# Kernel tuning notes

Hardware: AMD Instinct MI355X
Metric: run time of the kernel (lower is better)

Reference implementation:

```python
import jax, jax.numpy as jnp
import numpy as np

B, K, D = 128, 64, 1536        # batch, image regions, CNN feature dim
EM, H, A = 512, 1024, 1024     # embedding, hidden, attention dims
VOCAB, MAX_LEN = 10000, 30


def setup_inputs() -> dict:
    key = jax.random.key(0)
    ks = jax.random.split(key, 20)
    def p(i, shape):
        return jax.random.normal(ks[i], shape, dtype=jnp.float32) * 0.02
    z = lambda *s: jnp.zeros(s, jnp.float32)
    return {
        "im_input": jax.random.normal(ks[0], (B, K, D), dtype=jnp.float32),
        "w_input": jax.random.randint(ks[1], (B, MAX_LEN + 1), 0, VOCAB),
        "caption_lengths": jax.random.randint(ks[2], (B,), 2, MAX_LEN + 2),
        "emb": p(3, (VOCAB, EM)),
        "W_enc": p(4, (D, H)), "b_enc": z(H),
        "W_glob": p(5, (D, EM)), "b_glob": z(EM),
        "W_ih": p(6, (2 * EM, 4 * H)), "b_ih": z(4 * H),
        "W_hh": p(7, (H, 4 * H)), "b_hh": z(4 * H),
        "W_xg": p(8, (2 * EM, H)), "b_xg": z(H),
        "W_hg": p(9, (H, H)), "b_hg": z(H),
        "Wv": p(10, (H, A)), "bv": z(A),
        "Ws": p(11, (H, A)), "bs": z(A),
        "Wh": p(12, (H, A)), "bh": z(A),
        "wa": p(13, (A, 1)), "ba": z(1),
        "W_out": p(14, (H, VOCAB)), "b_out": z(VOCAB),
    }


def _forward(im_input, emb, W_enc, b_enc, W_glob, b_glob, W_ih, b_ih, W_hh, b_hh,
             W_xg, b_xg, W_hg, b_hg, Wv, bv, Ws, bs, Wh, bh, wa, ba, W_out, b_out,
             w_input, caption_lengths):
    # ImageEncoder: per-region features (B,K,H) and global feature (B,EM)
    V = jax.nn.relu(jnp.einsum('bkd,dh->bkh', im_input, W_enc) + b_enc)
    g = jax.nn.relu(jnp.mean(im_input, axis=1) @ W_glob + b_glob)
    # sort batch by caption length, descending (as in the torch forward)
    order = jnp.argsort(-caption_lengths)
    w = w_input[order]
    g = g[order]
    V = V[order]
    lens = caption_lengths[order] - 1  # has_end_seq_token=True
    target = w[:, 1:]
    h0 = jnp.zeros((B, H), jnp.float32)
    c0 = jnp.zeros((B, H), jnp.float32)

    # Full-batch scan is math-equivalent to the dynamic batch_size_t slicing:
    # lengths are sorted descending, so rows that go inactive never become
    # active again; their masked predictions stay zero, matching the original.
    def step(carry, t):
        h, c = carry
        x = jnp.concatenate([emb[w[:, t]], g], axis=1)  # (B, 2*EM)
        # SentinelLSTM: standard LSTM cell + visual sentinel gate
        gates = x @ W_ih + b_ih + h @ W_hh + b_hh
        i_g, f_g, g_g, o_g = jnp.split(gates, 4, axis=1)
        c_new = jax.nn.sigmoid(f_g) * c + jax.nn.sigmoid(i_g) * jnp.tanh(g_g)
        h_new = jax.nn.sigmoid(o_g) * jnp.tanh(c_new)
        s = jax.nn.sigmoid(x @ W_xg + b_xg + h @ W_hg + b_hg) * jnp.tanh(c_new)
        # Adaptive attention over K regions + sentinel
        hp = h_new @ Wh + bh                                      # (B,A)
        zv = (jnp.tanh(V @ Wv + bv + hp[:, None, :]) @ wa)[..., 0] + ba  # (B,K)
        zs = jnp.tanh(s @ Ws + bs + hp) @ wa + ba                  # (B,1)
        alpha = jax.nn.softmax(jnp.concatenate([zv, zs], axis=1), axis=1)  # (B,K+1)
        ctx = jnp.einsum('bk,bkh->bh', alpha[:, :-1], V)
        beta = alpha[:, -1:]
        z_t = beta * s + (1.0 - beta) * ctx + h_new
        # MultimodalDecoder (decoding_stack_size=1 -> single projection)
        probs = jax.nn.softmax(z_t @ W_out + b_out, axis=1)        # (B,VOCAB)
        probs = jnp.where((t < lens)[:, None], probs, 0.0)
        return (h_new, c_new), probs

    _, P = jax.lax.scan(step, (h0, c0), jnp.arange(MAX_LEN))
    predictions = jnp.transpose(P, (1, 0, 2))  # (B, MAX_LEN, VOCAB)
    return predictions, target, lens


def reference(im_input, w_input, caption_lengths, emb, W_enc, b_enc, W_glob, b_glob,
              W_ih, b_ih, W_hh, b_hh, W_xg, b_xg, W_hg, b_hg, Wv, bv, Ws, bs,
              Wh, bh, wa, ba, W_out, b_out):
    return _forward(im_input, emb, W_enc, b_enc, W_glob, b_glob, W_ih, b_ih,
                    W_hh, b_hh, W_xg, b_xg, W_hg, b_hg, Wv, bv, Ws, bs, Wh, bh,
                    wa, ba, W_out, b_out, w_input, caption_lengths)
```

## Files before the change

kernel.cpp:

```cpp
#include <hip/hip_runtime.h>
#include <math.h>

#define NB 128
#define NKK 64
#define ND 1536
#define NEM 512
#define NH 1024
#define NVOC 10000
#define NT 30
#define CHT 6

#define BM 128
#define BN 64
#define BK 64

typedef __bf16 bf16x8 __attribute__((ext_vector_type(8)));
typedef __bf16 bf16x4 __attribute__((ext_vector_type(4)));
typedef float f32x4 __attribute__((ext_vector_type(4)));

__device__ __forceinline__ float ftanh(float x) {
    float e = __expf(2.f * x);
    return 1.f - 2.f * __builtin_amdgcn_rcpf(e + 1.f);
}
__device__ __forceinline__ float fsig(float x) {
    return __builtin_amdgcn_rcpf(1.f + __expf(-x));
}

__global__ void sort_kernel(const int* __restrict__ cap, const int* __restrict__ w,
                            float* __restrict__ out_target, float* __restrict__ out_lens,
                            int* __restrict__ order, int* __restrict__ lens_s,
                            int* __restrict__ widx) {
    __shared__ int lcap[NB];
    __shared__ int sord[NB];
    int b = threadIdx.x;
    lcap[b] = cap[b];
    __syncthreads();
    int lb = lcap[b];
    int pos = 0;
    for (int j = 0; j < NB; j++) {
        int lj = lcap[j];
        if (lj > lb || (lj == lb && j < b)) pos++;
    }
    sord[pos] = b;
    __syncthreads();
    int src = sord[b];
    order[b] = src;
    int ln = lcap[src] - 1;
    lens_s[b] = ln;
    out_lens[b] = (float)ln;
    for (int j = 0; j < NT; j++)
        out_target[b * NT + j] = (float)w[src * (NT + 1) + j + 1];
    for (int t = 0; t < NT; t++)
        widx[t * NB + b] = w[src * (NT + 1) + t];
}

__global__ void init_kernel(float* __restrict__ c, float* __restrict__ ghh0,
                            float* __restrict__ ghh1) {
    int tid = blockIdx.x * 256 + threadIdx.x;
    if (tid < NB * NH) c[tid] = 0.f;
    if (tid < NB * 5120) { ghh0[tid] = 0.f; ghh1[tid] = 0.f; }
}

__global__ void meanim_kernel(const float* __restrict__ im, const int* __restrict__ order,
                              __bf16* __restrict__ meanb) {
    int b = blockIdx.x;
    int src = order[b];
    const float* base = im + (size_t)src * NKK * ND;
    for (int d = threadIdx.x; d < ND; d += 256) {
        float acc = 0.f;
        for (int k = 0; k < NKK; k++) acc += base[(size_t)k * ND + d];
        meanb[b * ND + d] = (__bf16)(acc * (1.0f / NKK));
    }
}

__global__ void conv_perm_kernel(const float* __restrict__ im, const int* __restrict__ order,
                                 __bf16* __restrict__ imb) {
    int e8 = blockIdx.x * 256 + threadIdx.x;
    size_t elem = (size_t)e8 * 8;
    int bp = (int)(elem / (NKK * ND));
    size_t rem = elem % (NKK * ND);
    const float* src = im + (size_t)order[bp] * NKK * ND + rem;
    float4 f0 = *(const float4*)(src);
    float4 f1 = *(const float4*)(src + 4);
    bf16x8 v = {(__bf16)f0.x, (__bf16)f0.y, (__bf16)f0.z, (__bf16)f0.w,
                (__bf16)f1.x, (__bf16)f1.y, (__bf16)f1.z, (__bf16)f1.w};
    *(bf16x8*)(imb + elem) = v;
}

__global__ __launch_bounds__(256) void transpose_pack(
    const float* __restrict__ src, int ldn, int K, int N,
    __bf16* __restrict__ dst, int ldk) {
    __shared__ float tile[64][65];
    int k0 = blockIdx.y * 64, n0 = blockIdx.x * 64;
    int t = threadIdx.x;
    int kr = t >> 2, nc0 = (t & 3) * 16;
    int kk = k0 + kr;
#pragma unroll
    for (int j = 0; j < 16; j += 4) {
        int nn = n0 + nc0 + j;
        float4 v = make_float4(0.f, 0.f, 0.f, 0.f);
        if (kk < K && nn + 3 < N) v = *(const float4*)(src + (size_t)kk * ldn + nn);
        else if (kk < K) {
            float tmp[4] = {0.f, 0.f, 0.f, 0.f};
            for (int q = 0; q < 4; q++) if (nn + q < N) tmp[q] = src[(size_t)kk * ldn + nn + q];
            v = make_float4(tmp[0], tmp[1], tmp[2], tmp[3]);
        }
        tile[kr][nc0 + j + 0] = v.x; tile[kr][nc0 + j + 1] = v.y;
        tile[kr][nc0 + j + 2] = v.z; tile[kr][nc0 + j + 3] = v.w;
    }
    __syncthreads();
    int nr = t >> 2, kc0 = (t & 3) * 16;
    if (n0 + nr < N) {
        __bf16* drow = dst + (size_t)(n0 + nr) * ldk + k0 + kc0;
#pragma unroll
        for (int j = 0; j < 16; j++)
            if (k0 + kc0 + j < K) drow[j] = (__bf16)tile[kc0 + j][nr];
    }
}

__global__ void conv_bf16_vec(const float* __restrict__ src, __bf16* __restrict__ dst, int n4) {
    int id = blockIdx.x * 256 + threadIdx.x;
    if (id < n4) {
        float4 v = *(const float4*)(src + (size_t)id * 4);
        __bf16* d = dst + (size_t)id * 4;
        d[0] = (__bf16)v.x; d[1] = (__bf16)v.y; d[2] = (__bf16)v.z; d[3] = (__bf16)v.w;
    }
}

__global__ void pack_biases(const float* __restrict__ b_ih, const float* __restrict__ b_hh,
                            const float* __restrict__ b_xg, const float* __restrict__ b_hg,
                            const float* __restrict__ bh, const float* __restrict__ bs,
                            float* __restrict__ bstep, float* __restrict__ b2) {
    int i = blockIdx.x * 256 + threadIdx.x;
    if (i < 4096) bstep[i] = b_ih[i] + b_hh[i];
    else bstep[i] = b_xg[i - 4096] + b_hg[i - 4096];
    if (i < 1024) b2[i] = bh[i];
    else if (i < 2048) b2[i] = bs[i - 1024];
}

template <int AMODE, bool RELU, bool OUTBF>
__global__ __launch_bounds__(256) void gemm_k(
    const void* __restrict__ Aptr, int lda,
    const __bf16* __restrict__ Bt, int ldb,
    const float* __restrict__ bias,
    void* __restrict__ Cptr, int ldc,
    int N, int K,
    const int* __restrict__ widx,
    const __bf16* __restrict__ embb, const __bf16* __restrict__ gbf,
    int swz, size_t sA, size_t sB, size_t sBias, size_t sC) {
    const int t = threadIdx.x;
    const int lane = t & 63;
    const int wid = t >> 6;
    const int wr = wid >> 1, wc = wid & 1;
    int bx = blockIdx.x, by = blockIdx.y;
    if (swz == 1) {
        int L = by * gridDim.x + bx;
        int xcd = L & 7, q = L >> 3;
        by = xcd * (gridDim.y >> 3) + q / gridDim.x;
        bx = q % gridDim.x;
    } else if (swz == 3) {
        int total = gridDim.x * gridDim.y;
        int L = by * gridDim.x + bx;
        int xcd = L & 7, idx = L >> 3;
        int newL = xcd * (total >> 3) + idx;
        by = newL / gridDim.x;
        bx = newL % gridDim.x;
    }
    const int z = blockIdx.z;
    const int m0 = by * BM;
    const int n0 = bx * BN;
    const int lr = lane & 15, lg = lane >> 4, lr8 = lr & 7;

    __shared__ __bf16 As[BM * BK];
    __shared__ __bf16 Bs[BN * BK];

    f32x4 acc[4][2];
#pragma unroll
    for (int i = 0; i < 4; i++)
#pragma unroll
        for (int j = 0; j < 2; j++) acc[i][j] = (f32x4){0.f, 0.f, 0.f, 0.f};

    const int s_row = t >> 1;
    const int s_g0 = (t & 1) * 4;
    const int s_col = t >> 2;
    const int s_bg0 = (t & 3) * 2;
    const int r8 = s_row & 7, c8 = s_col & 7;
    const int aw0 = (s_row << 6) + (((s_g0 + 0) ^ r8) << 3);
    const int aw1 = (s_row << 6) + (((s_g0 + 1) ^ r8) << 3);
    const int aw2 = (s_row << 6) + (((s_g0 + 2) ^ r8) << 3);
    const int aw3 = (s_row << 6) + (((s_g0 + 3) ^ r8) << 3);
    const int bw0 = (s_col << 6) + (((s_bg0 + 0) ^ c8) << 3);
    const int bw1 = (s_col << 6) + (((s_bg0 + 1) ^ c8) << 3);
    const int rA0 = (wr * 64 + 0 * 16 + lr) << 6;
    const int rA1 = (wr * 64 + 1 * 16 + lr) << 6;
    const int rA2 = (wr * 64 + 2 * 16 + lr) << 6;
    const int rA3 = (wr * 64 + 3 * 16 + lr) << 6;
    const int cB0 = (wc * 32 + 0 * 16 + lr) << 6;
    const int cB1 = (wc * 32 + 1 * 16 + lr) << 6;

    const __bf16* a_srcb = nullptr;
    const __bf16* e_base = nullptr;
    const __bf16* g_base = nullptr;
    if (AMODE == 1) {
        int r = m0 + s_row;
        e_base = embb + (size_t)widx[r] * NEM + s_g0 * 8;
        g_base = gbf + (size_t)(r & 127) * NEM + s_g0 * 8 - NEM;
    } else {
        a_srcb = (const __bf16*)Aptr + z * sA + (size_t)(m0 + s_row) * lda + s_g0 * 8;
    }
    const __bf16* b_src = Bt + z * sB + (size_t)(n0 + s_col) * ldb + s_bg0 * 8;
    const bool b_ok = (n0 + s_col) < N;

    auto loadA = [&](int k0, bf16x8& a0, bf16x8& a1, bf16x8& a2, bf16x8& a3) {
        if (AMODE == 1) {
            int kk = k0 + s_g0 * 8;
            const bf16x8* p = (const bf16x8*)((kk < NEM ? e_base : g_base) + k0);
            a0 = p[0]; a1 = p[1]; a2 = p[2]; a3 = p[3];
        } else {
            const bf16x8* p = (const bf16x8*)(a_srcb + k0);
            a0 = p[0]; a1 = p[1]; a2 = p[2]; a3 = p[3];
        }
    };
    auto loadB = [&](int k0, bf16x8& b0, bf16x8& b1) {
        if (b_ok) {
            const bf16x8* p = (const bf16x8*)(b_src + k0);
            b0 = p[0]; b1 = p[1];
        } else {
            bf16x8 zv = {};
            b0 = zv; b1 = zv;
        }
    };
    auto writeS = [&](bf16x8 a0, bf16x8 a1, bf16x8 a2, bf16x8 a3, bf16x8 b0, bf16x8 b1) {
        *(bf16x8*)&As[aw0] = a0; *(bf16x8*)&As[aw1] = a1;
        *(bf16x8*)&As[aw2] = a2; *(bf16x8*)&As[aw3] = a3;
        *(bf16x8*)&Bs[bw0] = b0; *(bf16x8*)&Bs[bw1] = b1;
    };
    auto compute = [&]() {
#pragma unroll
        for (int ks = 0; ks < 2; ks++) {
            const int gsw = ((ks * 4 + lg) ^ lr8) << 3;
            bf16x8 af0 = *(const bf16x8*)&As[rA0 + gsw];
            bf16x8 af1 = *(const bf16x8*)&As[rA1 + gsw];
            bf16x8 af2 = *(const bf16x8*)&As[rA2 + gsw];
            bf16x8 af3 = *(const bf16x8*)&As[rA3 + gsw];
            bf16x8 bv0 = *(const bf16x8*)&Bs[cB0 + gsw];
            bf16x8 bv1 = *(const bf16x8*)&Bs[cB1 + gsw];
            acc[0][0] = __builtin_amdgcn_mfma_f32_16x16x32_bf16(af0, bv0, acc[0][0], 0, 0, 0);
            acc[0][1] = __builtin_amdgcn_mfma_f32_16x16x32_bf16(af0, bv1, acc[0][1], 0, 0, 0);
            acc[1][0] = __builtin_amdgcn_mfma_f32_16x16x32_bf16(af1, bv0, acc[1][0], 0, 0, 0);
            acc[1][1] = __builtin_amdgcn_mfma_f32_16x16x32_bf16(af1, bv1, acc[1][1], 0, 0, 0);
            acc[2][0] = __builtin_amdgcn_mfma_f32_16x16x32_bf16(af2, bv0, acc[2][0], 0, 0, 0);
            acc[2][1] = __builtin_amdgcn_mfma_f32_16x16x32_bf16(af2, bv1, acc[2][1], 0, 0, 0);
            acc[3][0] = __builtin_amdgcn_mfma_f32_16x16x32_bf16(af3, bv0, acc[3][0], 0, 0, 0);
            acc[3][1] = __builtin_amdgcn_mfma_f32_16x16x32_bf16(af3, bv1, acc[3][1], 0, 0, 0);
        }
    };

    bf16x8 a0, a1, a2, a3, b0, b1;
    bf16x8 c0, c1, c2, c3, d0, d1;
    loadA(0, a0, a1, a2, a3);
    loadB(0, b0, b1);
    for (int k0 = 0; k0 < K; k0 += 2 * BK) {
        writeS(a0, a1, a2, a3, b0, b1);
        __syncthreads();
        loadA(k0 + BK, c0, c1, c2, c3);
        loadB(k0 + BK, d0, d1);
        compute();
        __syncthreads();
        writeS(c0, c1, c2, c3, d0, d1);
        __syncthreads();
        if (k0 + 2 * BK < K) {
            loadA(k0 + 2 * BK, a0, a1, a2, a3);
            loadB(k0 + 2 * BK, b0, b1);
        }
        compute();
        __syncthreads();
    }

    const float* bias_z = bias + z * sBias;
    float* Cf = (float*)Cptr + z * sC;
    __bf16* Cb = (__bf16*)Cptr + z * sC;
#pragma unroll
    for (int mi = 0; mi < 4; mi++) {
#pragma unroll
        for (int ni = 0; ni < 2; ni++) {
            int col = n0 + wc * 32 + ni * 16 + lr;
            if (col < N) {
                float bb = bias_z[col];
#pragma unroll
                for (int rr = 0; rr < 4; rr++) {
                    int row = m0 + wr * 64 + mi * 16 + lg * 4 + rr;
                    float v = acc[mi][ni][rr] + bb;
                    if (RELU) v = fmaxf(v, 0.f);
                    if (OUTBF) Cb[(size_t)row * ldc + col] = (__bf16)v;
                    else Cf[(size_t)row * ldc + col] = v;
                }
            }
        }
    }
}

__device__ __forceinline__ void step_gemm(
    __bf16* As, __bf16* Bs,
    const __bf16* __restrict__ Ab, int lda,
    const __bf16* __restrict__ Bt, int ldb,
    const float* __restrict__ bias,
    float* __restrict__ C, int ldc, int N, int n0, int K) {
    const int t = threadIdx.x;
    const int lane = t & 63;
    const int wid = t >> 6;
    const int wr = wid >> 1, wc = wid & 1;
    const int lr = lane & 15, lg = lane >> 4, lr8 = lr & 7;

    f32x4 acc[4][2];
#pragma unroll
    for (int i = 0; i < 4; i++)
#pragma unroll
        for (int j = 0; j < 2; j++) acc[i][j] = (f32x4){0.f, 0.f, 0.f, 0.f};

    const int s_row = t >> 1;
    const int s_g0 = (t & 1) * 4;
    const int s_col = t >> 2;
    const int s_bg0 = (t & 3) * 2;
    const int r8 = s_row & 7, c8 = s_col & 7;
    const int aw0 = (s_row << 6) + (((s_g0 + 0) ^ r8) << 3);
    const int aw1 = (s_row << 6) + (((s_g0 + 1) ^ r8) << 3);
    const int aw2 = (s_row << 6) + (((s_g0 + 2) ^ r8) << 3);
    const int aw3 = (s_row << 6) + (((s_g0 + 3) ^ r8) << 3);
    const int bw0 = (s_col << 6) + (((s_bg0 + 0) ^ c8) << 3);
    const int bw1 = (s_col << 6) + (((s_bg0 + 1) ^ c8) << 3);
    const int rA0 = (wr * 64 + 0 * 16 + lr) << 6;
    const int rA1 = (wr * 64 + 1 * 16 + lr) << 6;
    const int rA2 = (wr * 64 + 2 * 16 + lr) << 6;
    const int rA3 = (wr * 64 + 3 * 16 + lr) << 6;
    const int cB0 = (wc * 32 + 0 * 16 + lr) << 6;
    const int cB1 = (wc * 32 + 1 * 16 + lr) << 6;

    const __bf16* a_src = Ab + (size_t)s_row * lda + s_g0 * 8;
    const __bf16* b_src = Bt + (size_t)(n0 + s_col) * ldb + s_bg0 * 8;
    const bool b_ok = (n0 + s_col) < N;

    auto loadA = [&](int k0, bf16x8& a0, bf16x8& a1, bf16x8& a2, bf16x8& a3) {
        const bf16x8* p = (const bf16x8*)(a_src + k0);
        a0 = p[0]; a1 = p[1]; a2 = p[2]; a3 = p[3];
    };
    auto loadB = [&](int k0, bf16x8& b0, bf16x8& b1) {
        if (b_ok) {
            const bf16x8* p = (const bf16x8*)(b_src + k0);
            b0 = p[0]; b1 = p[1];
        } else {
            bf16x8 zv = {};
            b0 = zv; b1 = zv;
        }
    };
    auto writeS = [&](bf16x8 a0, bf16x8 a1, bf16x8 a2, bf16x8 a3, bf16x8 b0, bf16x8 b1) {
        *(bf16x8*)&As[aw0] = a0; *(bf16x8*)&As[aw1] = a1;
        *(bf16x8*)&As[aw2] = a2; *(bf16x8*)&As[aw3] = a3;
        *(bf16x8*)&Bs[bw0] = b0; *(bf16x8*)&Bs[bw1] = b1;
    };
    auto compute = [&]() {
#pragma unroll
        for (int ks = 0; ks < 2; ks++) {
            const int gsw = ((ks * 4 + lg) ^ lr8) << 3;
            bf16x8 af0 = *(const bf16x8*)&As[rA0 + gsw];
            bf16x8 af1 = *(const bf16x8*)&As[rA1 + gsw];
            bf16x8 af2 = *(const bf16x8*)&As[rA2 + gsw];
            bf16x8 af3 = *(const bf16x8*)&As[rA3 + gsw];
            bf16x8 bv0 = *(const bf16x8*)&Bs[cB0 + gsw];
            bf16x8 bv1 = *(const bf16x8*)&Bs[cB1 + gsw];
            acc[0][0] = __builtin_amdgcn_mfma_f32_16x16x32_bf16(af0, bv0, acc[0][0], 0, 0, 0);
            acc[0][1] = __builtin_amdgcn_mfma_f32_16x16x32_bf16(af0, bv1, acc[0][1], 0, 0, 0);
            acc[1][0] = __builtin_amdgcn_mfma_f32_16x16x32_bf16(af1, bv0, acc[1][0], 0, 0, 0);
            acc[1][1] = __builtin_amdgcn_mfma_f32_16x16x32_bf16(af1, bv1, acc[1][1], 0, 0, 0);
            acc[2][0] = __builtin_amdgcn_mfma_f32_16x16x32_bf16(af2, bv0, acc[2][0], 0, 0, 0);
            acc[2][1] = __builtin_amdgcn_mfma_f32_16x16x32_bf16(af2, bv1, acc[2][1], 0, 0, 0);
            acc[3][0] = __builtin_amdgcn_mfma_f32_16x16x32_bf16(af3, bv0, acc[3][0], 0, 0, 0);
            acc[3][1] = __builtin_amdgcn_mfma_f32_16x16x32_bf16(af3, bv1, acc[3][1], 0, 0, 0);
        }
    };

    bf16x8 a0, a1, a2, a3, b0, b1;
    bf16x8 c0, c1, c2, c3, d0, d1;
    loadA(0, a0, a1, a2, a3);
    loadB(0, b0, b1);
    for (int k0 = 0; k0 < K; k0 += 2 * BK) {
        writeS(a0, a1, a2, a3, b0, b1);
        __syncthreads();
        loadA(k0 + BK, c0, c1, c2, c3);
        loadB(k0 + BK, d0, d1);
        compute();
        __syncthreads();
        writeS(c0, c1, c2, c3, d0, d1);
        __syncthreads();
        if (k0 + 2 * BK < K) {
            loadA(k0 + 2 * BK, a0, a1, a2, a3);
            loadB(k0 + 2 * BK, b0, b1);
        }
        compute();
        __syncthreads();
    }

#pragma unroll
    for (int mi = 0; mi < 4; mi++) {
#pragma unroll
        for (int ni = 0; ni < 2; ni++) {
            int col = n0 + wc * 32 + ni * 16 + lr;
            if (col < N) {
                float bb = bias ? bias[col] : 0.f;
#pragma unroll
                for (int rr = 0; rr < 4; rr++) {
                    int row = wr * 64 + mi * 16 + lg * 4 + rr;
                    C[(size_t)row * ldc + col] = acc[mi][ni][rr] + bb;
                }
            }
        }
    }
}

__global__ __launch_bounds__(256) void lstm_kernel(
    const __bf16* __restrict__ Xpre, const float* __restrict__ g0,
    const float* __restrict__ g1, float* __restrict__ c,
    __bf16* __restrict__ H_all, __bf16* __restrict__ S_all, int t) {
    int i4 = (blockIdx.x * 256 + threadIdx.x) * 4;
    int b = i4 >> 10, j = i4 & 1023;
    const __bf16* xp = Xpre + ((size_t)t * NB + b) * 5120 + j;
    const float* p0 = g0 + (size_t)b * 5120 + j;
    const float* p1 = g1 + (size_t)b * 5120 + j;
    bf16x4 xi = *(const bf16x4*)(xp);
    bf16x4 xf = *(const bf16x4*)(xp + 1024);
    bf16x4 xg = *(const bf16x4*)(xp + 2048);
    bf16x4 xo = *(const bf16x4*)(xp + 3072);
    bf16x4 xs = *(const bf16x4*)(xp + 4096);
    float4 gi0 = *(const float4*)(p0), gi1 = *(const float4*)(p1);
    float4 gf0 = *(const float4*)(p0 + 1024), gf1 = *(const float4*)(p1 + 1024);
    float4 gg0 = *(const float4*)(p0 + 2048), gg1 = *(const float4*)(p1 + 2048);
    float4 go0 = *(const float4*)(p0 + 3072), go1 = *(const float4*)(p1 + 3072);
    float4 gs0 = *(const float4*)(p0 + 4096), gs1 = *(const float4*)(p1 + 4096);
    float4 cv = *(const float4*)(c + i4);
    float ia[4] = {gi0.x + gi1.x, gi0.y + gi1.y, gi0.z + gi1.z, gi0.w + gi1.w};
    float fa[4] = {gf0.x + gf1.x, gf0.y + gf1.y, gf0.z + gf1.z, gf0.w + gf1.w};
    float ga[4] = {gg0.x + gg1.x, gg0.y + gg1.y, gg0.z + gg1.z, gg0.w + gg1.w};
    float oa[4] = {go0.x + go1.x, go0.y + go1.y, go0.z + go1.z, go0.w + go1.w};
    float sa[4] = {gs0.x + gs1.x, gs0.y + gs1.y, gs0.z + gs1.z, gs0.w + gs1.w};
    float cvp[4] = {cv.x, cv.y, cv.z, cv.w};
    float cn4[4];
    bf16x4 hv, sv;
#pragma unroll
    for (int e = 0; e < 4; e++) {
        float ig = fsig((float)xi[e] + ia[e]);
        float fg = fsig((float)xf[e] + fa[e]);
        float gv = ftanh((float)xg[e] + ga[e]);
        float og = fsig((float)xo[e] + oa[e]);
        float sg = fsig((float)xs[e] + sa[e]);
        float cn = fg * cvp[e] + ig * gv;
        float tc = ftanh(cn);
        cn4[e] = cn;
        hv[e] = (__bf16)(og * tc);
        sv[e] = (__bf16)(sg * tc);
    }
    *(float4*)(c + i4) = make_float4(cn4[0], cn4[1], cn4[2], cn4[3]);
    *(bf16x4*)(H_all + (size_t)t * NB * NH + i4) = hv;
    *(bf16x4*)(S_all + (size_t)t * NB * NH + i4) = sv;
}

__global__ __launch_bounds__(256) void gatesHH_kernel(
    const __bf16* __restrict__ H_t, const __bf16* __restrict__ Whh,
    float* __restrict__ g0, float* __restrict__ g1) {
    __shared__ __bf16 As[BM * BK];
    __shared__ __bf16 Bs[BN * BK];
    int kc = blockIdx.x & 1, n = blockIdx.x >> 1;
    step_gemm(As, Bs, H_t + kc * 512, NH, Whh + kc * 512, 2048, nullptr,
              kc == 0 ? g0 : g1, 5120, 5120, n * 64, 512);
}

__global__ __launch_bounds__(256) void attn_all_kernel(
    const __bf16* __restrict__ VA, const __bf16* __restrict__ V,
    const __bf16* __restrict__ HPa, const __bf16* __restrict__ SWSa,
    const float* __restrict__ wa, const __bf16* __restrict__ H_all,
    const __bf16* __restrict__ S_all, __bf16* __restrict__ Z_all) {
    __shared__ float zscore[NKK + 1];
    __shared__ float alpha_s[NKK + 1];
    int tb = blockIdx.x;
    int b = tb & 127;
    int wave = threadIdx.x >> 6, lane = threadIdx.x & 63;

    float hp_reg[16], wa_reg[16];
    {
        const bf16x8* hr = (const bf16x8*)(HPa + (size_t)tb * NH + lane * 16);
        bf16x8 h0 = hr[0], h1 = hr[1];
        const float* wb = wa + lane * 16;
#pragma unroll
        for (int q = 0; q < 4; q++) {
            float4 wv = *(const float4*)(wb + q * 4);
            wa_reg[q * 4 + 0] = wv.x; wa_reg[q * 4 + 1] = wv.y;
            wa_reg[q * 4 + 2] = wv.z; wa_reg[q * 4 + 3] = wv.w;
        }
#pragma unroll
        for (int j = 0; j < 8; j++) { hp_reg[j] = (float)h0[j]; hp_reg[8 + j] = (float)h1[j]; }
    }
    for (int k = wave; k <= NKK; k += 4) {
        float p = 0.f;
        if (k < NKK) {
            const bf16x8* row = (const bf16x8*)(VA + ((size_t)(b * NKK + k)) * NH + lane * 16);
            bf16x8 v0 = row[0], v1 = row[1];
#pragma unroll
            for (int j = 0; j < 8; j++) {
                p += ftanh((float)v0[j] + hp_reg[j]) * wa_reg[j];
                p += ftanh((float)v1[j] + hp_reg[8 + j]) * wa_reg[8 + j];
            }
        } else {
            const bf16x8* sr = (const bf16x8*)(SWSa + (size_t)tb * NH + lane * 16);
            bf16x8 s0 = sr[0], s1 = sr[1];
#pragma unroll
            for (int j = 0; j < 8; j++) {
                p += ftanh((float)s0[j] + hp_reg[j]) * wa_reg[j];
                p += ftanh((float)s1[j] + hp_reg[8 + j]) * wa_reg[8 + j];
            }
        }
        for (int off = 32; off; off >>= 1) p += __shfl_down(p, off);
        if (lane == 0) zscore[k] = p;
    }
    __syncthreads();
    if (threadIdx.x == 0) {
        float mx = zscore[0];
        for (int i = 1; i <= NKK; i++) mx = fmaxf(mx, zscore[i]);
        float ssum = 0.f;
        for (int i = 0; i <= NKK; i++) { float e = __expf(zscore[i] - mx); alpha_s[i] = e; ssum += e; }
        float inv = __builtin_amdgcn_rcpf(ssum);
        for (int i = 0; i <= NKK; i++) alpha_s[i] *= inv;
    }
    __syncthreads();
    float beta = alpha_s[NKK];
    {
        int jj0 = threadIdx.x * 4;
        const __bf16* vp = V + ((size_t)b * NKK) * NH + jj0;
        float c0 = 0.f, c1 = 0.f, c2 = 0.f, c3 = 0.f;
#pragma unroll 8
        for (int k = 0; k < NKK; k++) {
            bf16x4 vv = *(const bf16x4*)(vp + (size_t)k * NH);
            float a = alpha_s[k];
            c0 += a * (float)vv[0]; c1 += a * (float)vv[1];
            c2 += a * (float)vv[2]; c3 += a * (float)vv[3];
        }
        bf16x4 s4 = *(const bf16x4*)(S_all + (size_t)tb * NH + jj0);
        bf16x4 h4 = *(const bf16x4*)(H_all + (size_t)tb * NH + jj0);
        float ob = 1.f - beta;
        bf16x4 zv;
        zv[0] = (__bf16)(beta * (float)s4[0] + ob * c0 + (float)h4[0]);
        zv[1] = (__bf16)(beta * (float)s4[1] + ob * c1 + (float)h4[1]);
        zv[2] = (__bf16)(beta * (float)s4[2] + ob * c2 + (float)h4[2]);
        zv[3] = (__bf16)(beta * (float)s4[3] + ob * c3 + (float)h4[3]);
        *(bf16x4*)(Z_all + (size_t)tb * NH + jj0) = zv;
    }
}

__global__ __launch_bounds__(256) void softmax_chunk_kernel(
    const float* __restrict__ logitsC, const int* __restrict__ lens,
    float* __restrict__ pred, int t0) {
    __shared__ float se[NVOC];
    __shared__ float sred[4], sred2[4];
    int r = blockIdx.x;
    int tt = r >> 7, b = r & 127;
    int t = t0 + tt;
    float* out = pred + (size_t)b * NT * NVOC + (size_t)t * NVOC;
    if (t >= lens[b]) {
        for (int v = threadIdx.x; v < NVOC; v += 256) out[v] = 0.f;
        return;
    }
    const float* lg = logitsC + (size_t)r * NVOC;
    float mx = -1e30f;
    for (int v = threadIdx.x; v < NVOC; v += 256) {
        float x = lg[v];
        se[v] = x;
        mx = fmaxf(mx, x);
    }
    for (int off = 32; off; off >>= 1) mx = fmaxf(mx, __shfl_down(mx, off));
    if ((threadIdx.x & 63) == 0) sred[threadIdx.x >> 6] = mx;
    __syncthreads();
    mx = fmaxf(fmaxf(sred[0], sred[1]), fmaxf(sred[2], sred[3]));
    float ssum = 0.f;
    for (int v = threadIdx.x; v < NVOC; v += 256) {
        float e = __expf(se[v] - mx);
        se[v] = e;
        ssum += e;
    }
    for (int off = 32; off; off >>= 1) ssum += __shfl_down(ssum, off);
    if ((threadIdx.x & 63) == 0) sred2[threadIdx.x >> 6] = ssum;
    __syncthreads();
    ssum = sred2[0] + sred2[1] + sred2[2] + sred2[3];
    float inv = 1.f / ssum;
    for (int v = threadIdx.x; v < NVOC; v += 256) out[v] = se[v] * inv;
}

extern "C" void kernel_launch(void* const* d_in, const int* in_sizes, int n_in,
                              void* d_out, int out_size, void* d_ws, size_t ws_size,
                              hipStream_t stream) {
    const float* im = (const float*)d_in[0];
    const int* w_in = (const int*)d_in[1];
    const int* cap = (const int*)d_in[2];
    const float* emb = (const float*)d_in[3];
    const float* W_enc = (const float*)d_in[4];
    const float* b_enc = (const float*)d_in[5];
    const float* W_glob = (const float*)d_in[6];
    const float* b_glob = (const float*)d_in[7];
    const float* W_ih = (const float*)d_in[8];
    const float* b_ih = (const float*)d_in[9];
    const float* W_hh = (const float*)d_in[10];
    const float* b_hh = (const float*)d_in[11];
    const float* W_xg = (const float*)d_in[12];
    const float* b_xg = (const float*)d_in[13];
    const float* W_hg = (const float*)d_in[14];
    const float* b_hg = (const float*)d_in[15];
    const float* Wv = (const float*)d_in[16];
    const float* bv = (const float*)d_in[17];
    const float* Ws = (const float*)d_in[18];
    const float* bs = (const float*)d_in[19];
    const float* Wh = (const float*)d_in[20];
    const float* bh = (const float*)d_in[21];
    const float* wa = (const float*)d_in[22];
    const float* W_out = (const float*)d_in[24];
    const float* b_out = (const float*)d_in[25];

    float* out = (float*)d_out;
    float* pred = out;
    float* out_target = out + (size_t)NB * NT * NVOC;
    float* out_lens = out_target + NB * NT;

    char* p = (char*)d_ws;
    size_t off = 0;
    auto carve = [&](size_t bytes) {
        void* r = p + off;
        off += (bytes + 255) & ~(size_t)255;
        return r;
    };
    int* order = (int*)carve(NB * 4);
    int* lens_s = (int*)carve(NB * 4);
    int* widx = (int*)carve(NT * NB * 4);
    __bf16* embb = (__bf16*)carve((size_t)NVOC * NEM * 2);
    __bf16* Wstep_t = (__bf16*)carve((size_t)5120 * 2048 * 2);
    __bf16* W2t = (__bf16*)carve((size_t)2 * 1024 * 1024 * 2);
    __bf16* Wout_t = (__bf16*)carve((size_t)NVOC * 1024 * 2);
    __bf16* Wglob_t = (__bf16*)carve((size_t)512 * 1536 * 2);
    __bf16* Wenc_t = (__bf16*)carve((size_t)1024 * 1536 * 2);
    __bf16* Wv_t = (__bf16*)carve((size_t)1024 * 1024 * 2);
    float* bstep = (float*)carve(5120 * 4);
    float* b2 = (float*)carve(2048 * 4);
    __bf16* meanb = (__bf16*)carve((size_t)NB * ND * 2);
    __bf16* g_bf = (__bf16*)carve((size_t)NB * NEM * 2);
    __bf16* V_bf = (__bf16*)carve((size_t)NB * NKK * NH * 2);
    __bf16* VA_bf = (__bf16*)carve((size_t)NB * NKK * NH * 2);
    void* uni = carve((size_t)NT * NB * 5120 * 2);
    __bf16* imb = (__bf16*)uni;
    __bf16* Xpre = (__bf16*)uni;
    float* logitsC = (float*)uni;
    float* ghh0 = (float*)carve((size_t)NB * 5120 * 4);
    float* ghh1 = (float*)carve((size_t)NB * 5120 * 4);
    float* c = (float*)carve((size_t)NB * NH * 4);
    __bf16* H_all = (__bf16*)carve((size_t)NT * NB * NH * 2);
    __bf16* S_all = (__bf16*)carve((size_t)NT * NB * NH * 2);
    __bf16* HPa = (__bf16*)carve((size_t)NT * NB * NH * 2);
    __bf16* SWSa = (__bf16*)carve((size_t)NT * NB * NH * 2);
    __bf16* Z_all = (__bf16*)carve((size_t)NT * NB * NH * 2);
    if (off > ws_size) return;
    size_t off_save = off;
    float* logitsF = (float*)carve((size_t)NT * NB * NVOC * 4);
    bool useFull = (off <= ws_size);
    if (!useFull) off = off_save;

    sort_kernel<<<1, NB, 0, stream>>>(cap, w_in, out_target, out_lens, order, lens_s, widx);
    init_kernel<<<(NB * 5120 + 255) / 256, 256, 0, stream>>>(c, ghh0, ghh1);
    pack_biases<<<20, 256, 0, stream>>>(b_ih, b_hh, b_xg, b_hg, bh, bs, bstep, b2);
    conv_bf16_vec<<<(NVOC * NEM / 4 + 255) / 256, 256, 0, stream>>>(emb, embb, NVOC * NEM / 4);
    transpose_pack<<<dim3(8, 24), 256, 0, stream>>>(W_glob, 512, 1536, 512, Wglob_t, 1536);
    transpose_pack<<<dim3(16, 24), 256, 0, stream>>>(W_enc, 1024, 1536, 1024, Wenc_t, 1536);
    transpose_pack<<<dim3(16, 16), 256, 0, stream>>>(Wv, 1024, 1024, 1024, Wv_t, 1024);
    transpose_pack<<<dim3(64, 16), 256, 0, stream>>>(W_ih, 4096, 1024, 4096, Wstep_t, 2048);
    transpose_pack<<<dim3(64, 16), 256, 0, stream>>>(W_hh, 4096, 1024, 4096, Wstep_t + 1024, 2048);
    transpose_pack<<<dim3(16, 16), 256, 0, stream>>>(W_xg, 1024, 1024, 1024,
                                                     Wstep_t + (size_t)4096 * 2048, 2048);
    transpose_pack<<<dim3(16, 16), 256, 0, stream>>>(W_hg, 1024, 1024, 1024,
                                                     Wstep_t + (size_t)4096 * 2048 + 1024, 2048);
    transpose_pack<<<dim3(16, 16), 256, 0, stream>>>(Wh, 1024, 1024, 1024, W2t, 1024);
    transpose_pack<<<dim3(16, 16), 256, 0, stream>>>(Ws, 1024, 1024, 1024,
                                                     W2t + (size_t)1024 * 1024, 1024);
    transpose_pack<<<dim3(157, 16), 256, 0, stream>>>(W_out, NVOC, 1024, NVOC, Wout_t, 1024);
    meanim_kernel<<<NB, 256, 0, stream>>>(im, order, meanb);
    conv_perm_kernel<<<(NB * NKK * ND / 8) / 256, 256, 0, stream>>>(im, order, imb);

    gemm_k<0, true, true><<<dim3(NEM / BN, 1), 256, 0, stream>>>(
        meanb, ND, Wglob_t, ND, b_glob, g_bf, NEM, NEM, ND, nullptr, nullptr, nullptr,
        0, 0, 0, 0, 0);
    gemm_k<0, true, true><<<dim3(NH / BN, (NB * NKK) / BM), 256, 0, stream>>>(
        imb, ND, Wenc_t, ND, b_enc, V_bf, NH, NH, ND, nullptr, nullptr, nullptr,
        1, 0, 0, 0, 0);
    gemm_k<0, false, true><<<dim3(NH / BN, (NB * NKK) / BM), 256, 0, stream>>>(
        V_bf, NH, Wv_t, NH, bv, VA_bf, NH, NH, NH, nullptr, nullptr, nullptr,
        1, 0, 0, 0, 0);
    gemm_k<1, false, true><<<dim3(5120 / BN, (NT * NB) / BM), 256, 0, stream>>>(
        nullptr, 0, Wstep_t, 2048, bstep, Xpre, 5120, 5120, 1024, widx, embb, g_bf,
        3, 0, 0, 0, 0);

    for (int t = 0; t < NT; t++) {
        lstm_kernel<<<128, 256, 0, stream>>>(Xpre, ghh0, ghh1, c, H_all, S_all, t);
        if (t < NT - 1)
            gatesHH_kernel<<<160, 256, 0, stream>>>(
                H_all + (size_t)t * NB * NH, Wstep_t + 1024, ghh0, ghh1);
    }

    gemm_k<0, false, true><<<dim3(NH / BN, NT, 2), 256, 0, stream>>>(
        H_all, NH, W2t, NH, b2, HPa, NH, NH, NH, nullptr, nullptr, nullptr,
        3, (size_t)NT * NB * NH, (size_t)NH * NH, (size_t)NH, (size_t)NT * NB * NH);
    attn_all_kernel<<<NT * NB, 256, 0, stream>>>(VA_bf, V_bf, HPa, SWSa, wa, H_all, S_all, Z_all);

    if (useFull) {
        gemm_k<0, false, false><<<dim3(160, NT), 256, 0, stream>>>(
            Z_all, NH, Wout_t, NH, b_out, logitsF, NVOC, NVOC, NH, nullptr, nullptr, nullptr,
            3, 0, 0, 0, 0);
        softmax_chunk_kernel<<<NT * NB, 256, 0, stream>>>(logitsF, lens_s, pred, 0);
    } else {
        for (int c5 = 0; c5 < NT / CHT; c5++) {
            gemm_k<0, false, false><<<dim3(160, CHT), 256, 0, stream>>>(
                Z_all + (size_t)c5 * CHT * NB * NH, NH, Wout_t, NH, b_out, logitsC, NVOC,
                NVOC, NH, nullptr, nullptr, nullptr, 3, 0, 0, 0, 0);
            softmax_chunk_kernel<<<CHT * NB, 256, 0, stream>>>(logitsC, lens_s, pred, c5 * CHT);
        }
    }
}
```

Baseline: 1.054 ms.

## Compact live timesteps for output GEMM and split recurrent K four ways

Builds a compacted list of live (t,b) rows in the sort kernel and uses it to gather Z rows for the vocab projection, so blocks past the live count exit early and the softmax reads logits through a row map. Attention blocks for masked positions now return immediately. The per-step recurrent gate GEMM splits K into four partials instead of two, which doubles the grid for more parallelism, and the LSTM kernel sums four partial buffers. The cost is extra partial-buffer traffic and zero-initialisation, plus an indirect row gather in the GEMM.

```diff
diff --git a/kernel.cpp b/kernel.cpp
--- a/kernel.cpp
+++ b/kernel.cpp
@@ -29,9 +29,11 @@
 __global__ void sort_kernel(const int* __restrict__ cap, const int* __restrict__ w,
                             float* __restrict__ out_target, float* __restrict__ out_lens,
                             int* __restrict__ order, int* __restrict__ lens_s,
-                            int* __restrict__ widx) {
+                            int* __restrict__ widx, int* __restrict__ live_tb,
+                            int* __restrict__ row_of, int* __restrict__ counts) {
     __shared__ int lcap[NB];
     __shared__ int sord[NB];
+    __shared__ int slen[NB];
     int b = threadIdx.x;
     lcap[b] = cap[b];
     __syncthreads();
@@ -47,18 +49,32 @@
     order[b] = src;
     int ln = lcap[src] - 1;
     lens_s[b] = ln;
+    slen[b] = ln;
     out_lens[b] = (float)ln;
     for (int j = 0; j < NT; j++)
         out_target[b * NT + j] = (float)w[src * (NT + 1) + j + 1];
     for (int t = 0; t < NT; t++)
         widx[t * NB + b] = w[src * (NT + 1) + t];
-}
-
-__global__ void init_kernel(float* __restrict__ c, float* __restrict__ ghh0,
-                            float* __restrict__ ghh1) {
+    __syncthreads();
+    int prefix = 0;
+    for (int j = 0; j < b; j++) prefix += slen[j];
+    for (int t = 0; t < ln; t++) {
+        row_of[t * NB + b] = prefix + t;
+        live_tb[prefix + t] = t * NB + b;
+    }
+    if (b == NB - 1) {
+        int nLive = prefix + ln;
+        counts[0] = nLive;
+        counts[1] = (nLive + BM - 1) & ~(BM - 1);
+    }
+}
+
+__global__ void init_kernel(float* __restrict__ c, float* __restrict__ g0,
+                            float* __restrict__ g1, float* __restrict__ g2,
+                            float* __restrict__ g3) {
     int tid = blockIdx.x * 256 + threadIdx.x;
     if (tid < NB * NH) c[tid] = 0.f;
-    if (tid < NB * 5120) { ghh0[tid] = 0.f; ghh1[tid] = 0.f; }
+    if (tid < NB * 5120) { g0[tid] = 0.f; g1[tid] = 0.f; g2[tid] = 0.f; g3[tid] = 0.f; }
 }
 
 __global__ void meanim_kernel(const float* __restrict__ im, const int* __restrict__ order,
@@ -147,7 +163,8 @@
     int N, int K,
     const int* __restrict__ widx,
     const __bf16* __restrict__ embb, const __bf16* __restrict__ gbf,
-    int swz, size_t sA, size_t sB, size_t sBias, size_t sC) {
+    int swz, size_t sA, size_t sB, size_t sBias, size_t sC,
+    const int* __restrict__ live_tb, const int* __restrict__ cnts) {
     const int t = threadIdx.x;
     const int lane = t & 63;
     const int wid = t >> 6;
@@ -169,6 +186,7 @@
     const int z = blockIdx.z;
     const int m0 = by * BM;
     const int n0 = bx * BN;
+    if (AMODE == 2 && m0 >= cnts[1]) return;
     const int lr = lane & 15, lg = lane >> 4, lr8 = lr & 7;
 
     __shared__ __bf16 As[BM * BK];
@@ -205,6 +223,11 @@
         int r = m0 + s_row;
         e_base = embb + (size_t)widx[r] * NEM + s_g0 * 8;
         g_base = gbf + (size_t)(r & 127) * NEM + s_g0 * 8 - NEM;
+    } else if (AMODE == 2) {
+        int r = m0 + s_row;
+        int nl = cnts[0];
+        int rr = r < nl ? r : nl - 1;
+        a_srcb = (const __bf16*)Aptr + (size_t)live_tb[rr] * lda + s_g0 * 8;
     } else {
         a_srcb = (const __bf16*)Aptr + z * sA + (size_t)(m0 + s_row) * lda + s_g0 * 8;
     }
@@ -419,44 +442,37 @@
 
 __global__ __launch_bounds__(256) void lstm_kernel(
     const __bf16* __restrict__ Xpre, const float* __restrict__ g0,
-    const float* __restrict__ g1, float* __restrict__ c,
+    const float* __restrict__ g1, const float* __restrict__ g2,
+    const float* __restrict__ g3, float* __restrict__ c,
     __bf16* __restrict__ H_all, __bf16* __restrict__ S_all, int t) {
     int i4 = (blockIdx.x * 256 + threadIdx.x) * 4;
     int b = i4 >> 10, j = i4 & 1023;
     const __bf16* xp = Xpre + ((size_t)t * NB + b) * 5120 + j;
-    const float* p0 = g0 + (size_t)b * 5120 + j;
-    const float* p1 = g1 + (size_t)b * 5120 + j;
-    bf16x4 xi = *(const bf16x4*)(xp);
-    bf16x4 xf = *(const bf16x4*)(xp + 1024);
-    bf16x4 xg = *(const bf16x4*)(xp + 2048);
-    bf16x4 xo = *(const bf16x4*)(xp + 3072);
-    bf16x4 xs = *(const bf16x4*)(xp + 4096);
-    float4 gi0 = *(const float4*)(p0), gi1 = *(const float4*)(p1);
-    float4 gf0 = *(const float4*)(p0 + 1024), gf1 = *(const float4*)(p1 + 1024);
-    float4 gg0 = *(const float4*)(p0 + 2048), gg1 = *(const float4*)(p1 + 2048);
-    float4 go0 = *(const float4*)(p0 + 3072), go1 = *(const float4*)(p1 + 3072);
-    float4 gs0 = *(const float4*)(p0 + 4096), gs1 = *(const float4*)(p1 + 4096);
+    size_t gof = (size_t)b * 5120 + j;
     float4 cv = *(const float4*)(c + i4);
-    float ia[4] = {gi0.x + gi1.x, gi0.y + gi1.y, gi0.z + gi1.z, gi0.w + gi1.w};
-    float fa[4] = {gf0.x + gf1.x, gf0.y + gf1.y, gf0.z + gf1.z, gf0.w + gf1.w};
-    float ga[4] = {gg0.x + gg1.x, gg0.y + gg1.y, gg0.z + gg1.z, gg0.w + gg1.w};
-    float oa[4] = {go0.x + go1.x, go0.y + go1.y, go0.z + go1.z, go0.w + go1.w};
-    float sa[4] = {gs0.x + gs1.x, gs0.y + gs1.y, gs0.z + gs1.z, gs0.w + gs1.w};
     float cvp[4] = {cv.x, cv.y, cv.z, cv.w};
+    float pre[5][4];
+#pragma unroll
+    for (int q = 0; q < 5; q++) {
+        bf16x4 xv = *(const bf16x4*)(xp + q * 1024);
+        float4 a0 = *(const float4*)(g0 + gof + q * 1024);
+        float4 a1 = *(const float4*)(g1 + gof + q * 1024);
+        float4 a2 = *(const float4*)(g2 + gof + q * 1024);
+        float4 a3 = *(const float4*)(g3 + gof + q * 1024);
+        pre[q][0] = (float)xv[0] + a0.x + a1.x + a2.x + a3.x;
+        pre[q][1] = (float)xv[1] + a0.y + a1.y + a2.y + a3.y;
+        pre[q][2] = (float)xv[2] + a0.z + a1.z + a2.z + a3.z;
+        pre[q][3] = (float)xv[3] + a0.w + a1.w + a2.w + a3.w;
+    }
     float cn4[4];
     bf16x4 hv, sv;
 #pragma unroll
     for (int e = 0; e < 4; e++) {
-        float ig = fsig((float)xi[e] + ia[e]);
-        float fg = fsig((float)xf[e] + fa[e]);
-        float gv = ftanh((float)xg[e] + ga[e]);
-        float og = fsig((float)xo[e] + oa[e]);
-        float sg = fsig((float)xs[e] + sa[e]);
-        float cn = fg * cvp[e] + ig * gv;
+        float cn = fsig(pre[1][e]) * cvp[e] + fsig(pre[0][e]) * ftanh(pre[2][e]);
         float tc = ftanh(cn);
         cn4[e] = cn;
-        hv[e] = (__bf16)(og * tc);
-        sv[e] = (__bf16)(sg * tc);
+        hv[e] = (__bf16)(fsig(pre[3][e]) * tc);
+        sv[e] = (__bf16)(fsig(pre[4][e]) * tc);
     }
     *(float4*)(c + i4) = make_float4(cn4[0], cn4[1], cn4[2], cn4[3]);
     *(bf16x4*)(H_all + (size_t)t * NB * NH + i4) = hv;
@@ -465,23 +481,27 @@
 
 __global__ __launch_bounds__(256) void gatesHH_kernel(
     const __bf16* __restrict__ H_t, const __bf16* __restrict__ Whh,
-    float* __restrict__ g0, float* __restrict__ g1) {
+    float* __restrict__ g0, float* __restrict__ g1,
+    float* __restrict__ g2, float* __restrict__ g3) {
     __shared__ __bf16 As[BM * BK];
     __shared__ __bf16 Bs[BN * BK];
-    int kc = blockIdx.x & 1, n = blockIdx.x >> 1;
-    step_gemm(As, Bs, H_t + kc * 512, NH, Whh + kc * 512, 2048, nullptr,
-              kc == 0 ? g0 : g1, 5120, 5120, n * 64, 512);
+    int kc = blockIdx.x & 3, n = blockIdx.x >> 2;
+    float* outp = (kc == 0) ? g0 : (kc == 1) ? g1 : (kc == 2) ? g2 : g3;
+    step_gemm(As, Bs, H_t + kc * 256, NH, Whh + kc * 256, 2048, nullptr,
+              outp, 5120, 5120, n * 64, 256);
 }
 
 __global__ __launch_bounds__(256) void attn_all_kernel(
     const __bf16* __restrict__ VA, const __bf16* __restrict__ V,
     const __bf16* __restrict__ HPa, const __bf16* __restrict__ SWSa,
     const float* __restrict__ wa, const __bf16* __restrict__ H_all,
-    const __bf16* __restrict__ S_all, __bf16* __restrict__ Z_all) {
+    const __bf16* __restrict__ S_all, __bf16* __restrict__ Z_all,
+    const int* __restrict__ lens) {
     __shared__ float zscore[NKK + 1];
     __shared__ float alpha_s[NKK + 1];
     int tb = blockIdx.x;
     int b = tb & 127;
+    if ((tb >> 7) >= lens[b]) return;
     int wave = threadIdx.x >> 6, lane = threadIdx.x & 63;
 
     float hp_reg[16], wa_reg[16];
@@ -554,9 +574,10 @@
     }
 }
 
-__global__ __launch_bounds__(256) void softmax_chunk_kernel(
-    const float* __restrict__ logitsC, const int* __restrict__ lens,
-    float* __restrict__ pred, int t0) {
+template <bool COMPACT>
+__global__ __launch_bounds__(256) void softmax_kernel(
+    const float* __restrict__ logitsB, const int* __restrict__ lens,
+    const int* __restrict__ row_of, float* __restrict__ pred, int t0) {
     __shared__ float se[NVOC];
     __shared__ float sred[4], sred2[4];
     int r = blockIdx.x;
@@ -567,7 +588,8 @@
         for (int v = threadIdx.x; v < NVOC; v += 256) out[v] = 0.f;
         return;
     }
-    const float* lg = logitsC + (size_t)r * NVOC;
+    size_t srcrow = COMPACT ? (size_t)row_of[t * NB + b] : (size_t)r;
+    const float* lg = logitsB + srcrow * NVOC;
     float mx = -1e30f;
     for (int v = threadIdx.x; v < NVOC; v += 256) {
         float x = lg[v];
@@ -636,6 +658,9 @@
     int* order = (int*)carve(NB * 4);
     int* lens_s = (int*)carve(NB * 4);
     int* widx = (int*)carve(NT * NB * 4);
+    int* live_tb = (int*)carve(NT * NB * 4);
+    int* row_of = (int*)carve(NT * NB * 4);
+    int* counts = (int*)carve(2 * 4);
     __bf16* embb = (__bf16*)carve((size_t)NVOC * NEM * 2);
     __bf16* Wstep_t = (__bf16*)carve((size_t)5120 * 2048 * 2);
     __bf16* W2t = (__bf16*)carve((size_t)2 * 1024 * 1024 * 2);
@@ -655,6 +680,8 @@
     float* logitsC = (float*)uni;
     float* ghh0 = (float*)carve((size_t)NB * 5120 * 4);
     float* ghh1 = (float*)carve((size_t)NB * 5120 * 4);
+    float* ghh2 = (float*)carve((size_t)NB * 5120 * 4);
+    float* ghh3 = (float*)carve((size_t)NB * 5120 * 4);
     float* c = (float*)carve((size_t)NB * NH * 4);
     __bf16* H_all = (__bf16*)carve((size_t)NT * NB * NH * 2);
     __bf16* S_all = (__bf16*)carve((size_t)NT * NB * NH * 2);
@@ -667,8 +694,9 @@
     bool useFull = (off <= ws_size);
     if (!useFull) off = off_save;
 
-    sort_kernel<<<1, NB, 0, stream>>>(cap, w_in, out_target, out_lens, order, lens_s, widx);
-    init_kernel<<<(NB * 5120 + 255) / 256, 256, 0, stream>>>(c, ghh0, ghh1);
+    sort_kernel<<<1, NB, 0, stream>>>(cap, w_in, out_target, out_lens, order, lens_s, widx,
+                                      live_tb, row_of, counts);
+    init_kernel<<<(NB * 5120 + 255) / 256, 256, 0, stream>>>(c, ghh0, ghh1, ghh2, ghh3);
     pack_biases<<<20, 256, 0, stream>>>(b_ih, b_hh, b_xg, b_hg, bh, bs, bstep, b2);
     conv_bf16_vec<<<(NVOC * NEM / 4 + 255) / 256, 256, 0, stream>>>(emb, embb, NVOC * NEM / 4);
     transpose_pack<<<dim3(8, 24), 256, 0, stream>>>(W_glob, 512, 1536, 512, Wglob_t, 1536);
@@ -689,40 +717,43 @@
 
     gemm_k<0, true, true><<<dim3(NEM / BN, 1), 256, 0, stream>>>(
         meanb, ND, Wglob_t, ND, b_glob, g_bf, NEM, NEM, ND, nullptr, nullptr, nullptr,
-        0, 0, 0, 0, 0);
+        0, 0, 0, 0, 0, nullptr, nullptr);
     gemm_k<0, true, true><<<dim3(NH / BN, (NB * NKK) / BM), 256, 0, stream>>>(
         imb, ND, Wenc_t, ND, b_enc, V_bf, NH, NH, ND, nullptr, nullptr, nullptr,
-        1, 0, 0, 0, 0);
+        1, 0, 0, 0, 0, nullptr, nullptr);
     gemm_k<0, false, true><<<dim3(NH / BN, (NB * NKK) / BM), 256, 0, stream>>>(
         V_bf, NH, Wv_t, NH, bv, VA_bf, NH, NH, NH, nullptr, nullptr, nullptr,
-        1, 0, 0, 0, 0);
+        1, 0, 0, 0, 0, nullptr, nullptr);
     gemm_k<1, false, true><<<dim3(5120 / BN, (NT * NB) / BM), 256, 0, stream>>>(
         nullptr, 0, Wstep_t, 2048, bstep, Xpre, 5120, 5120, 1024, widx, embb, g_bf,
-        3, 0, 0, 0, 0);
+        3, 0, 0, 0, 0, nullptr, nullptr);
 
     for (int t = 0; t < NT; t++) {
-        lstm_kernel<<<128, 256, 0, stream>>>(Xpre, ghh0, ghh1, c, H_all, S_all, t);
+        lstm_kernel<<<128, 256, 0, stream>>>(Xpre, ghh0, ghh1, ghh2, ghh3, c, H_all, S_all, t);
         if (t < NT - 1)
-            gatesHH_kernel<<<160, 256, 0, stream>>>(
-                H_all + (size_t)t * NB * NH, Wstep_t + 1024, ghh0, ghh1);
+            gatesHH_kernel<<<320, 256, 0, stream>>>(
+                H_all + (size_t)t * NB * NH, Wstep_t + 1024, ghh0, ghh1, ghh2, ghh3);
     }
 
     gemm_k<0, false, true><<<dim3(NH / BN, NT, 2), 256, 0, stream>>>(
         H_all, NH, W2t, NH, b2, HPa, NH, NH, NH, nullptr, nullptr, nullptr,
-        3, (size_t)NT * NB * NH, (size_t)NH * NH, (size_t)NH, (size_t)NT * NB * NH);
-    attn_all_kernel<<<NT * NB, 256, 0, stream>>>(VA_bf, V_bf, HPa, SWSa, wa, H_all, S_all, Z_all);
+        3, (size_t)NT * NB * NH, (size_t)NH * NH, (size_t)NH, (size_t)NT * NB * NH,
+        nullptr, nullptr);
+    attn_all_kernel<<<NT * NB, 256, 0, stream>>>(VA_bf, V_bf, HPa, SWSa, wa, H_all, S_all,
+                                                 Z_all, lens_s);
 
     if (useFull) {
-        gemm_k<0, false, false><<<dim3(160, NT), 256, 0, stream>>>(
+        gemm_k<2, false, false><<<dim3(160, NT), 256, 0, stream>>>(
             Z_all, NH, Wout_t, NH, b_out, logitsF, NVOC, NVOC, NH, nullptr, nullptr, nullptr,
-            3, 0, 0, 0, 0);
-        softmax_chunk_kernel<<<NT * NB, 256, 0, stream>>>(logitsF, lens_s, pred, 0);
+            3, 0, 0, 0, 0, live_tb, counts);
+        softmax_kernel<true><<<NT * NB, 256, 0, stream>>>(logitsF, lens_s, row_of, pred, 0);
     } else {
         for (int c5 = 0; c5 < NT / CHT; c5++) {
             gemm_k<0, false, false><<<dim3(160, CHT), 256, 0, stream>>>(
                 Z_all + (size_t)c5 * CHT * NB * NH, NH, Wout_t, NH, b_out, logitsC, NVOC,
-                NVOC, NH, nullptr, nullptr, nullptr, 3, 0, 0, 0, 0);
-            softmax_chunk_kernel<<<CHT * NB, 256, 0, stream>>>(logitsC, lens_s, pred, c5 * CHT);
-        }
-    }
-}
+                NVOC, NH, nullptr, nullptr, nullptr, 3, 0, 0, 0, 0, nullptr, nullptr);
+            softmax_kernel<false><<<CHT * NB, 256, 0, stream>>>(logitsC, lens_s, nullptr, pred,
+                                                                c5 * CHT);
+        }
+    }
+}
```

Result: no change. 1.054 ms (+0.0%).
